# Kernel optimization log

Hardware: AMD Instinct MI355X
Metric: run time of the kernel (lower is better)

## Reference

```python
import jax, jax.numpy as jnp
import numpy as np

N, M, D = 16384, 1024, 1024


def setup_inputs() -> dict:
    key = jax.random.key(0)
    kq, kp = jax.random.split(key)
    query = jax.random.normal(kq, (N, D), dtype=jnp.float32)
    proto = jax.random.normal(kp, (M, D), dtype=jnp.float32)
    return {"query": query, "proto": proto}


def reference(query, proto):
    # Pairwise squared euclidean: ||q||^2 - 2 q.p + ||p||^2  (same math as
    # the expand+pow+sum in compute_euclidean, but without the [N,M,D] blowup).
    q2 = jnp.sum(query * query, axis=-1, keepdims=True)          # [N,1]
    p2 = jnp.sum(proto * proto, axis=-1)                          # [M]
    qp = jnp.einsum('nd,md->nm', query, proto)                    # [N,M]
    dists = q2 - 2.0 * qp + p2[None, :]                           # [N,M]
    # Original applies F.softmax(-dists, dim=1) (named log_p_y but is softmax).
    return jax.nn.softmax(-dists, axis=1)
```

## Files before the change

### kernel.cpp

```cpp
#include <hip/hip_runtime.h>
#include <stdint.h>

#define N_Q 16384
#define M_P 1024
#define D_K 1024

typedef __attribute__((ext_vector_type(8))) __bf16 bf16x8;
typedef __attribute__((ext_vector_type(4))) float floatx4;
typedef __attribute__((ext_vector_type(4))) unsigned int uint4v;

#define AS1 __attribute__((address_space(1)))
#define AS3 __attribute__((address_space(3)))

__device__ __forceinline__ unsigned short f2bf(float f) {
    unsigned int u = __float_as_uint(f);
    u += 0x7fffu + ((u >> 16) & 1u);
    return (unsigned short)(u >> 16);
}
__device__ __forceinline__ float bf2f(unsigned short h) {
    return __uint_as_float(((unsigned int)h) << 16);
}

__device__ __forceinline__ void split_chunk(floatx4 f0, floatx4 f1,
                                            uint4v* hi, uint4v* lo) {
    float e[8] = {f0.x, f0.y, f0.z, f0.w, f1.x, f1.y, f1.z, f1.w};
    unsigned int hb[4], lb[4];
#pragma unroll
    for (int p = 0; p < 4; ++p) {
        unsigned int u0 = __float_as_uint(e[2 * p]);
        unsigned int u1 = __float_as_uint(e[2 * p + 1]);
        hb[p] = __builtin_amdgcn_perm(u1, u0, 0x07060302);
        float l0 = e[2 * p]     - __uint_as_float(u0 & 0xffff0000u);
        float l1 = e[2 * p + 1] - __uint_as_float(u1 & 0xffff0000u);
        lb[p] = __builtin_amdgcn_perm(__float_as_uint(l1), __float_as_uint(l0),
                                      0x07060302);
    }
    uint4v h = {hb[0], hb[1], hb[2], hb[3]};
    uint4v l = {lb[0], lb[1], lb[2], lb[3]};
    *hi = h;
    *lo = l;
}

__global__ __launch_bounds__(256) void convert_proto_kernel(
    const float* __restrict__ proto, unsigned short* __restrict__ ph,
    unsigned short* __restrict__ pl, float* __restrict__ p2) {
    __shared__ float sred[4];
    int m = blockIdx.x;
    int t = threadIdx.x;
    size_t base4 = (size_t)m * (D_K / 4) + t;
    float4 v = ((const float4*)proto)[base4];
    ushort4 h, l;
    h.x = f2bf(v.x); l.x = f2bf(v.x - bf2f(h.x));
    h.y = f2bf(v.y); l.y = f2bf(v.y - bf2f(h.y));
    h.z = f2bf(v.z); l.z = f2bf(v.z - bf2f(h.z));
    h.w = f2bf(v.w); l.w = f2bf(v.w - bf2f(h.w));
    ((ushort4*)ph)[base4] = h;
    ((ushort4*)pl)[base4] = l;
    float sq = v.x * v.x + v.y * v.y + v.z * v.z + v.w * v.w;
#pragma unroll
    for (int off = 1; off < 64; off <<= 1) sq += __shfl_xor(sq, off);
    if ((t & 63) == 0) sred[t >> 6] = sq;
    __syncthreads();
    if (t == 0) p2[m] = sred[0] + sred[1] + sred[2] + sred[3];
}

__global__ __launch_bounds__(512, 2) void gemm_logits_kernel(
    const float* __restrict__ query,
    const unsigned short* __restrict__ ph, const unsigned short* __restrict__ pl,
    const float* __restrict__ p2, float* __restrict__ out) {
    __shared__ unsigned short sAh[2][16 * 512];
    __shared__ unsigned short sAl[2][16 * 512];
    __shared__ unsigned short sBh[2][16 * 512];
    __shared__ unsigned short sBl[2][16 * 512];

    const int tid = threadIdx.x;
    const int wave = tid >> 6;
    const int lane = tid & 63;
    const int wr = wave >> 2;
    const int wc = wave & 3;

    const int b = blockIdx.x;
    const int v = (b & 7) * 32 + (b >> 3);
    const int colt = v >> 6;
    const int rowt = v & 63;
    const int row0 = rowt * 256;
    const int col0 = colt * 256;

    const int rlB = lane >> 2;
    const int cioB = (lane & 3) ^ ((lane >> 3) & 3);
    const int halfB = wave >> 2;
    const int sgB = wave & 3;
    const unsigned short* gB = (halfB ? pl : ph)
        + (size_t)(col0 + sgB * 64 + rlB) * D_K + cioB * 8;

    const int rlA = lane >> 2;
    const int cA = lane & 3;
    const AS1 float* gA = (const AS1 float*)query
        + (size_t)(row0 + wave * 32 + rlA) * D_K + cA * 8;
    const int wroff = (4 * rlA + (cA ^ ((rlA >> 1) & 3))) * 8;

    const int rsel = lane & 15;
    const int kq = lane >> 4;
    const int fragoff = (4 * rsel + (kq ^ ((rsel >> 1) & 3))) * 8;

    floatx4 zero = {0.0f, 0.0f, 0.0f, 0.0f};
    floatx4 acc[8][4];
#pragma unroll
    for (int i = 0; i < 8; ++i)
#pragma unroll
        for (int j = 0; j < 4; ++j) acc[i][j] = zero;

    floatx4 f0[2], f1[2];
    bf16x8 bh[4], bl[4];
    bf16x8 ah[2], al[2];

    auto issueA = [&](int kb) {
#pragma unroll
        for (int s = 0; s < 2; ++s) {
            const AS1 float* p = gA + (size_t)(s * 16) * D_K + kb;
            f0[s] = *(const AS1 floatx4*)p;
            f1[s] = *(const AS1 floatx4*)(p + 4);
        }
    };
    auto issueB = [&](int kb, int nxt) {
        unsigned short* dstB = (halfB ? sBl[nxt] : sBh[nxt]) + sgB * 4 * 512;
#pragma unroll
        for (int s = 0; s < 4; ++s)
            __builtin_amdgcn_global_load_lds(
                (const AS1 unsigned int*)(const void*)(gB + (size_t)(s * 16) * D_K + kb),
                (AS3 unsigned int*)(void*)(dstB + s * 512), 16, 0, 0);
    };
    auto writeA = [&](int nxt, int s) {
        uint4v hi, lo;
        split_chunk(f0[s], f1[s], &hi, &lo);
        const int off = (wave * 2 + s) * 512 + wroff;
        *(uint4v*)(sAh[nxt] + off) = hi;
        *(uint4v*)(sAl[nxt] + off) = lo;
    };
    auto ldBfrag = [&](int cur) {
#pragma unroll
        for (int j = 0; j < 4; ++j) {
            const int boff = (wc * 4 + j) * 512 + fragoff;
            bh[j] = *(const bf16x8*)(sBh[cur] + boff);
            bl[j] = *(const bf16x8*)(sBl[cur] + boff);
        }
    };
    auto ldAfrag = [&](int cur, int i0) {
#pragma unroll
        for (int t = 0; t < 2; ++t) {
            const int aoff = (wr * 8 + i0 + t) * 512 + fragoff;
            ah[t] = *(const bf16x8*)(sAh[cur] + aoff);
            al[t] = *(const bf16x8*)(sAl[cur] + aoff);
        }
    };
    auto mfma2 = [&](int i0) {
#pragma unroll
        for (int j = 0; j < 4; ++j)
#pragma unroll
            for (int t = 0; t < 2; ++t) {
                acc[i0 + t][j] = __builtin_amdgcn_mfma_f32_16x16x32_bf16(ah[t], bh[j], acc[i0 + t][j], 0, 0, 0);
                acc[i0 + t][j] = __builtin_amdgcn_mfma_f32_16x16x32_bf16(ah[t], bl[j], acc[i0 + t][j], 0, 0, 0);
                acc[i0 + t][j] = __builtin_amdgcn_mfma_f32_16x16x32_bf16(al[t], bh[j], acc[i0 + t][j], 0, 0, 0);
            }
    };

#define PHASE_MFMA(i0)                                          \
    __builtin_amdgcn_s_barrier();                               \
    asm volatile("s_waitcnt lgkmcnt(0)" ::: "memory");          \
    __builtin_amdgcn_sched_barrier(0);                          \
    __builtin_amdgcn_s_setprio(1);                              \
    mfma2(i0);                                                  \
    __builtin_amdgcn_s_setprio(0);                              \
    __builtin_amdgcn_s_barrier();

    auto stepf = [&](int kbnB, int kbnA, int cur, int nxt, bool pfB, bool pfA) {
        if (pfB) issueB(kbnB, nxt);
        ldBfrag(cur);
        ldAfrag(cur, 0);
        PHASE_MFMA(0)
        ldAfrag(cur, 2);
        PHASE_MFMA(2)
        ldAfrag(cur, 4);
        if (pfB) { writeA(nxt, 0); writeA(nxt, 1); }
        PHASE_MFMA(4)
        ldAfrag(cur, 6);
        if (pfA) issueA(kbnA);
        asm volatile("s_waitcnt lgkmcnt(0)" ::: "memory");
        if (pfB) {
            if (pfA) asm volatile("s_waitcnt vmcnt(4)" ::: "memory");
            else     asm volatile("s_waitcnt vmcnt(0)" ::: "memory");
        }
        __builtin_amdgcn_s_barrier();
        __builtin_amdgcn_sched_barrier(0);
        __builtin_amdgcn_s_setprio(1);
        mfma2(6);
        __builtin_amdgcn_s_setprio(0);
    };

    issueA(0);
    issueB(0, 0);
    writeA(0, 0);
    writeA(0, 1);
    issueA(32);
    asm volatile("s_waitcnt lgkmcnt(0)" ::: "memory");
    asm volatile("s_waitcnt vmcnt(4)" ::: "memory");
    __builtin_amdgcn_s_barrier();

    for (int kt = 0; kt < 30; kt += 2) {
        stepf((kt + 1) * 32, (kt + 2) * 32, 0, 1, true, true);
        stepf((kt + 2) * 32, (kt + 3) * 32, 1, 0, true, true);
    }
    stepf(31 * 32, 0, 0, 1, true, false);
    stepf(0, 0, 1, 0, false, false);

#undef PHASE_MFMA

#pragma unroll
    for (int j = 0; j < 4; ++j) {
        const int gc = col0 + wc * 64 + j * 16 + rsel;
        const float p2v = p2[gc];
#pragma unroll
        for (int i = 0; i < 8; ++i) {
            const int gr = row0 + wr * 128 + i * 16 + kq * 4;
#pragma unroll
            for (int r = 0; r < 4; ++r) {
                out[(size_t)(gr + r) * M_P + gc] = 2.0f * acc[i][j][r] - p2v;
            }
        }
    }
}

__global__ __launch_bounds__(256) void naive_logits_kernel(
    const float* __restrict__ query, const float* __restrict__ proto,
    float* __restrict__ out) {
    __shared__ float qs[D_K];
    int n = blockIdx.x;
    int t = threadIdx.x;
    ((float4*)qs)[t] = ((const float4*)(query + (size_t)n * D_K))[t];
    __syncthreads();
    float acc[4] = {0.f, 0.f, 0.f, 0.f};
    float pp[4] = {0.f, 0.f, 0.f, 0.f};
    for (int d = 0; d < D_K; d += 4) {
        float4 qv = *(const float4*)(qs + d);
#pragma unroll
        for (int j = 0; j < 4; ++j) {
            const float4 pv = *(const float4*)(proto + (size_t)(t + 256 * j) * D_K + d);
            acc[j] += qv.x * pv.x + qv.y * pv.y + qv.z * pv.z + qv.w * pv.w;
            pp[j] += pv.x * pv.x + pv.y * pv.y + pv.z * pv.z + pv.w * pv.w;
        }
    }
#pragma unroll
    for (int j = 0; j < 4; ++j)
        out[(size_t)n * M_P + t + 256 * j] = 2.0f * acc[j] - pp[j];
}

__global__ __launch_bounds__(256) void softmax_kernel(float* __restrict__ out) {
    const int lane = threadIdx.x & 63;
    int n = blockIdx.x * 4 + (threadIdx.x >> 6);
    for (int it = 0; it < 2; ++it, n += 8192) {
        float* row = out + (size_t)n * M_P;
        floatx4 v[4];
#pragma unroll
        for (int k = 0; k < 4; ++k)
            v[k] = *((const floatx4*)row + k * 64 + lane);
        float mx = fmaxf(fmaxf(v[0].x, v[0].y), fmaxf(v[0].z, v[0].w));
#pragma unroll
        for (int k = 1; k < 4; ++k)
            mx = fmaxf(mx, fmaxf(fmaxf(v[k].x, v[k].y), fmaxf(v[k].z, v[k].w)));
#pragma unroll
        for (int off = 1; off < 64; off <<= 1) mx = fmaxf(mx, __shfl_xor(mx, off));
        float s = 0.0f;
#pragma unroll
        for (int k = 0; k < 4; ++k) {
            v[k].x = __expf(v[k].x - mx);
            v[k].y = __expf(v[k].y - mx);
            v[k].z = __expf(v[k].z - mx);
            v[k].w = __expf(v[k].w - mx);
            s += v[k].x + v[k].y + v[k].z + v[k].w;
        }
#pragma unroll
        for (int off = 1; off < 64; off <<= 1) s += __shfl_xor(s, off);
        const float inv = 1.0f / s;
#pragma unroll
        for (int k = 0; k < 4; ++k) {
            floatx4 o;
            o.x = v[k].x * inv; o.y = v[k].y * inv;
            o.z = v[k].z * inv; o.w = v[k].w * inv;
            __builtin_nontemporal_store(o, (floatx4*)row + k * 64 + lane);
        }
    }
}

extern "C" void kernel_launch(void* const* d_in, const int* in_sizes, int n_in,
                              void* d_out, int out_size, void* d_ws, size_t ws_size,
                              hipStream_t stream) {
    const float* query = (const float*)d_in[0];
    const float* proto = (const float*)d_in[1];
    float* out = (float*)d_out;

    const size_t pElems = (size_t)M_P * D_K;
    const size_t needed = pElems * 2 * 2 + M_P * 4;

    if (ws_size >= needed) {
        unsigned short* ph = (unsigned short*)d_ws;
        unsigned short* pl = ph + pElems;
        float* p2 = (float*)(pl + pElems);

        convert_proto_kernel<<<M_P, 256, 0, stream>>>(proto, ph, pl, p2);
        gemm_logits_kernel<<<(N_Q / 256) * (M_P / 256), 512, 0, stream>>>(
            query, ph, pl, p2, out);
    } else {
        naive_logits_kernel<<<N_Q, 256, 0, stream>>>(query, proto, out);
    }
    softmax_kernel<<<2048, 256, 0, stream>>>(out);
}
```

Baseline: 202.0 us.

## Double-buffer A fragments and drop per-phase barriers in the MFMA main loop

```diff
diff --git a/kernel.cpp b/kernel.cpp
--- a/kernel.cpp
+++ b/kernel.cpp
@@ -112,7 +112,7 @@
 
     floatx4 f0[2], f1[2];
     bf16x8 bh[4], bl[4];
-    bf16x8 ah[2], al[2];
+    bf16x8 ah[2][2], al[2][2];
 
     auto issueA = [&](int kb) {
 #pragma unroll
@@ -145,56 +145,54 @@
             bl[j] = *(const bf16x8*)(sBl[cur] + boff);
         }
     };
-    auto ldAfrag = [&](int cur, int i0) {
+    auto ldA = [&](int cur, int i0, int set) {
 #pragma unroll
         for (int t = 0; t < 2; ++t) {
             const int aoff = (wr * 8 + i0 + t) * 512 + fragoff;
-            ah[t] = *(const bf16x8*)(sAh[cur] + aoff);
-            al[t] = *(const bf16x8*)(sAl[cur] + aoff);
-        }
-    };
-    auto mfma2 = [&](int i0) {
+            ah[set][t] = *(const bf16x8*)(sAh[cur] + aoff);
+            al[set][t] = *(const bf16x8*)(sAl[cur] + aoff);
+        }
+    };
+    auto mfma2 = [&](int i0, int set) {
 #pragma unroll
         for (int j = 0; j < 4; ++j)
 #pragma unroll
             for (int t = 0; t < 2; ++t) {
-                acc[i0 + t][j] = __builtin_amdgcn_mfma_f32_16x16x32_bf16(ah[t], bh[j], acc[i0 + t][j], 0, 0, 0);
-                acc[i0 + t][j] = __builtin_amdgcn_mfma_f32_16x16x32_bf16(ah[t], bl[j], acc[i0 + t][j], 0, 0, 0);
-                acc[i0 + t][j] = __builtin_amdgcn_mfma_f32_16x16x32_bf16(al[t], bh[j], acc[i0 + t][j], 0, 0, 0);
+                acc[i0 + t][j] = __builtin_amdgcn_mfma_f32_16x16x32_bf16(ah[set][t], bh[j], acc[i0 + t][j], 0, 0, 0);
+                acc[i0 + t][j] = __builtin_amdgcn_mfma_f32_16x16x32_bf16(ah[set][t], bl[j], acc[i0 + t][j], 0, 0, 0);
+                acc[i0 + t][j] = __builtin_amdgcn_mfma_f32_16x16x32_bf16(al[set][t], bh[j], acc[i0 + t][j], 0, 0, 0);
             }
     };
 
-#define PHASE_MFMA(i0)                                          \
-    __builtin_amdgcn_s_barrier();                               \
-    asm volatile("s_waitcnt lgkmcnt(0)" ::: "memory");          \
+#define LGKM_MFMA(n, i0, set)                                   \
+    asm volatile("s_waitcnt lgkmcnt(" #n ")" ::: "memory");     \
     __builtin_amdgcn_sched_barrier(0);                          \
     __builtin_amdgcn_s_setprio(1);                              \
-    mfma2(i0);                                                  \
-    __builtin_amdgcn_s_setprio(0);                              \
-    __builtin_amdgcn_s_barrier();
+    mfma2(i0, set);                                             \
+    __builtin_amdgcn_s_setprio(0);
 
     auto stepf = [&](int kbnB, int kbnA, int cur, int nxt, bool pfB, bool pfA) {
         if (pfB) issueB(kbnB, nxt);
         ldBfrag(cur);
-        ldAfrag(cur, 0);
-        PHASE_MFMA(0)
-        ldAfrag(cur, 2);
-        PHASE_MFMA(2)
-        ldAfrag(cur, 4);
+        ldA(cur, 0, 0);
+        ldA(cur, 2, 1);
+        LGKM_MFMA(4, 0, 0)
+        ldA(cur, 4, 0);
+        LGKM_MFMA(4, 2, 1)
+        ldA(cur, 6, 1);
+        LGKM_MFMA(4, 4, 0)
         if (pfB) { writeA(nxt, 0); writeA(nxt, 1); }
-        PHASE_MFMA(4)
-        ldAfrag(cur, 6);
         if (pfA) issueA(kbnA);
         asm volatile("s_waitcnt lgkmcnt(0)" ::: "memory");
         if (pfB) {
             if (pfA) asm volatile("s_waitcnt vmcnt(4)" ::: "memory");
             else     asm volatile("s_waitcnt vmcnt(0)" ::: "memory");
         }
-        __builtin_amdgcn_s_barrier();
         __builtin_amdgcn_sched_barrier(0);
         __builtin_amdgcn_s_setprio(1);
-        mfma2(6);
+        mfma2(6, 1);
         __builtin_amdgcn_s_setprio(0);
+        __builtin_amdgcn_s_barrier();
     };
 
     issueA(0);
@@ -213,7 +211,7 @@
     stepf(31 * 32, 0, 0, 1, true, false);
     stepf(0, 0, 1, 0, false, false);
 
-#undef PHASE_MFMA
+#undef LGKM_MFMA
 
 #pragma unroll
     for (int j = 0; j < 4; ++j) {
```

New measurement: 198.1 us. About the same (-1.9%).
